# Kernel optimization log

Hardware: AMD Instinct MI355X
Metric: run time of the kernel (lower is better)

Reference implementation:

```python
import jax, jax.numpy as jnp
import numpy as np

E = 16          # expert_num
T = 8192        # token_num
H = 1024        # hidden_size
I = 4096        # intermediate_size
LN_EPS = 1e-12


def setup_inputs() -> dict:
    key = jax.random.key(0)
    ks = jax.random.split(key, 6)
    hidden_states = jax.random.normal(ks[0], (T, H), dtype=jnp.float32)
    perm = jax.random.permutation(ks[1], T).astype(jnp.int32)
    s1 = 1.0 / np.sqrt(H)
    s2 = 1.0 / np.sqrt(I)
    w1 = jax.random.uniform(ks[2], (E, I, H), jnp.float32, -s1, s1)
    b1 = jax.random.uniform(ks[3], (E, I), jnp.float32, -s1, s1)
    w2 = jax.random.uniform(ks[4], (E, H, I), jnp.float32, -s2, s2)
    b2 = jax.random.uniform(ks[5], (E, H), jnp.float32, -s2, s2)
    ln_gamma = jnp.ones((H,), jnp.float32)
    ln_beta = jnp.zeros((H,), jnp.float32)
    return {"hidden_states": hidden_states, "perm": perm, "w1": w1, "b1": b1,
            "w2": w2, "b2": b2, "ln_gamma": ln_gamma, "ln_beta": ln_beta}


def _layer_norm(x, gamma, beta, eps):
    mu = jnp.mean(x, axis=-1, keepdims=True)
    var = jnp.var(x, axis=-1, keepdims=True)
    return (x - mu) * jax.lax.rsqrt(var + eps) * gamma + beta


def reference(hidden_states, perm, w1, b1, w2, b2, ln_gamma, ln_beta):
    # dispatch: gather tokens by random permutation, group per expert
    xp = hidden_states[perm].reshape(E, T // E, H)            # [E, T/E, H]
    # grouped expert FFN (batched GEMM replaces the per-expert Python loop)
    h = jnp.einsum('eth,eih->eti', xp, w1) + b1[:, None, :]   # [E, T/E, I]
    h = jax.nn.gelu(h, approximate=False)
    o = jnp.einsum('eti,ehi->eth', h, w2) + b2[:, None, :]    # [E, T/E, H]
    # scatter-restore via inverse permutation
    restore = jnp.argsort(perm)
    o = o.reshape(T, H)[restore]
    # dropout is identity (p=0, eval); residual + LayerNorm
    return _layer_norm(o + hidden_states, ln_gamma, ln_beta, LN_EPS)
```

## Files before the change

### kernel.cpp

```cpp
#include <hip/hip_runtime.h>
#include <hip/hip_bf16.h>
#include <stdint.h>

#define E_NUM 16
#define T_NUM 8192
#define H_DIM 1024
#define I_DIM 4096
#define MPE   512

typedef __attribute__((ext_vector_type(8))) short short8;
typedef __attribute__((ext_vector_type(4))) float f32x4;
using bf16 = __hip_bfloat16;

typedef const __attribute__((address_space(1))) void GLV;
typedef __attribute__((address_space(3))) void LDSV;

__device__ __forceinline__ uint32_t pack2_bf16(float a, float b) {
  union { float f; uint32_t u; } ua, ub;
  ua.f = a; ub.f = b;
  uint32_t x = ua.u + (0x7FFFu + ((ua.u >> 16) & 1u));
  uint32_t y = ub.u + (0x7FFFu + ((ub.u >> 16) & 1u));
  return (x >> 16) | (y & 0xFFFF0000u);
}

__device__ __forceinline__ short8 cvt8(f32x4 a, f32x4 b) {
  union { short8 s; __hip_bfloat162 h[4]; } r;
  r.h[0] = __float22bfloat162_rn({a[0], a[1]});
  r.h[1] = __float22bfloat162_rn({a[2], a[3]});
  r.h[2] = __float22bfloat162_rn({b[0], b[1]});
  r.h[3] = __float22bfloat162_rn({b[2], b[3]});
  return r.s;
}

__device__ __forceinline__ float fast_gelu(float x) {
  const float p = x * fmaf(x * x, -0.0713548162726f, -1.59576912161f);
  return x * __builtin_amdgcn_rcpf(1.0f + __expf(p));
}

__global__ __launch_bounds__(256)
void gather_cast_kernel(const float* __restrict__ hs, const int* __restrict__ perm,
                        uint32_t* __restrict__ xp) {
  const int r = blockIdx.x;
  const int t = threadIdx.x;
  const int src = perm[r];
  float4 v = ((const float4*)(hs + (size_t)src * H_DIM))[t];
  uint2 o;
  o.x = pack2_bf16(v.x, v.y);
  o.y = pack2_bf16(v.z, v.w);
  ((uint2*)(xp + (size_t)r * (H_DIM / 2)))[t] = o;
}

template<int LOG_NBN, int NWG>
__global__ __launch_bounds__(1024, 2)
void moe_gemm1_kernel(const bf16* __restrict__ A, const float* __restrict__ Bw,
                      const float* __restrict__ bias, bf16* __restrict__ Hout) {
  constexpr int N = I_DIM, K = H_DIM;
  constexpr int NK = K / 32;
  __shared__ bf16  As[2][512 * 32];
  __shared__ float Bs[2][64 * 32];

  constexpr int qx = NWG >> 3;
  const int orig = blockIdx.x;
  const int wg = (orig & 7) * qx + (orig >> 3);
  const int bn = wg & ((1 << LOG_NBN) - 1);
  const int e  = wg >> LOG_NBN;

  const int tid = threadIdx.x;
  const int l = tid & 63;
  const int w = tid >> 6;
  const int wr = w >> 1, wc = w & 1;
  const int fr = l & 15, fq = l >> 4;
  const int rx = fr & 7;

  const bf16*  Ae = A  + (size_t)e * MPE * K;
  const float* Be = Bw + ((size_t)e * N + (size_t)bn * 64) * K;

  const int apq = tid >> 3;
  const int ag  = (tid & 7) ^ (apq & 7);
  const bf16* As0 = Ae + (size_t)(apq       + 256 * (ag >> 2)) * K + (ag & 3) * 8;
  const bf16* As1 = Ae + (size_t)(apq + 128 + 256 * (ag >> 2)) * K + (ag & 3) * 8;

  const int brow = tid >> 3;
  const float* Bsrc = Be + (size_t)(brow & 63) * K + ((tid & 7) ^ (brow & 7)) * 4;

#define STAGE1(buf, kt)                                                            \
  {                                                                                \
    __builtin_amdgcn_global_load_lds((GLV*)(As0 + (kt) * 32),                      \
        (LDSV*)((char*)&As[buf][0] + tid * 16), 16, 0, 0);                         \
    __builtin_amdgcn_global_load_lds((GLV*)(As1 + (kt) * 32),                      \
        (LDSV*)((char*)&As[buf][0] + 16384 + tid * 16), 16, 0, 0);                 \
    if (tid < 512)                                                                 \
      __builtin_amdgcn_global_load_lds((GLV*)(Bsrc + (kt) * 32),                   \
          (LDSV*)((char*)&Bs[buf][0] + tid * 16), 16, 0, 0);                       \
  }

  const int aoff  = ((wr & 3) * 64 + fr) * 128 + ((((wr >> 2) << 2) | fq) ^ rx) * 16;
  const int b0off = (wc * 32 + fr) * 128 + (((fq << 1)) ^ rx) * 16;
  const int b1off = (wc * 32 + fr) * 128 + (((fq << 1) | 1) ^ rx) * 16;

  f32x4 acc[4][2];
#pragma unroll
  for (int m = 0; m < 4; ++m)
#pragma unroll
    for (int n = 0; n < 2; ++n) acc[m][n] = (f32x4){0.f, 0.f, 0.f, 0.f};

  STAGE1(0, 0);
  __syncthreads();

  for (int t = 0; t < NK; ++t) {
    const int cur = t & 1;
    if (t + 1 < NK) STAGE1(cur ^ 1, t + 1);

    short8 a8[4];
#pragma unroll
    for (int m = 0; m < 4; ++m)
      a8[m] = *(const short8*)((const char*)&As[cur][0] + aoff + m * 2048);
    short8 b8[2];
#pragma unroll
    for (int n = 0; n < 2; ++n) {
      const f32x4 x0 = *(const f32x4*)((const char*)&Bs[cur][0] + b0off + n * 2048);
      const f32x4 x1 = *(const f32x4*)((const char*)&Bs[cur][0] + b1off + n * 2048);
      b8[n] = cvt8(x0, x1);
    }
#pragma unroll
    for (int m = 0; m < 4; ++m)
#pragma unroll
      for (int n = 0; n < 2; ++n)
        acc[m][n] = __builtin_amdgcn_mfma_f32_16x16x32_bf16(a8[m], b8[n], acc[m][n], 0, 0, 0);

    __syncthreads();
  }
#undef STAGE1

  float bv[2];
#pragma unroll
  for (int n = 0; n < 2; ++n)
    bv[n] = bias[(size_t)e * N + bn * 64 + wc * 32 + n * 16 + fr];

  bf16* He = Hout + (size_t)e * MPE * N;
#pragma unroll
  for (int m = 0; m < 4; ++m) {
#pragma unroll
    for (int j = 0; j < 4; ++j) {
      const int row = wr * 64 + m * 16 + fq * 4 + j;
#pragma unroll
      for (int n = 0; n < 2; ++n) {
        const int col = bn * 64 + wc * 32 + n * 16 + fr;
        He[(size_t)row * N + col] = __float2bfloat16(fast_gelu(acc[m][n][j] + bv[n]));
      }
    }
  }
}

template<int KSPLIT, int N, int KFULL, int KLEN, int LOG_NBN>
__global__ __launch_bounds__(1024, 4)
void moe_gemm2_kernel(const bf16* __restrict__ A, const float* __restrict__ Bw,
                      float* __restrict__ Pout) {
  constexpr int NK = KLEN / 32;
  __shared__ bf16  As[2][512 * 32];
  __shared__ float Bs[2][128 * 32];

  const int nwg = gridDim.x, qx = nwg >> 3, orig = blockIdx.x;
  const int wg = (orig & 7) * qx + (orig >> 3);
  const int bn   = wg & ((1 << LOG_NBN) - 1);
  const int rest = wg >> LOG_NBN;
  const int ks = (KSPLIT == 2) ? (rest & 1) : 0;
  const int e  = (KSPLIT == 2) ? (rest >> 1) : rest;
  const int K0 = ks * KLEN;

  const int tid = threadIdx.x;
  const int l = tid & 63;
  const int w = tid >> 6;
  const int wr = w >> 1, wc = w & 1;
  const int fr = l & 15, fq = l >> 4;
  const int rx = fr & 7;

  const bf16*  Ae = A  + (size_t)e * MPE * KFULL + K0;
  const float* Be = Bw + ((size_t)e * N + (size_t)bn * 128) * KFULL + K0;

  const int apq = tid >> 3;
  const int ag  = (tid & 7) ^ (apq & 7);
  const bf16* As0 = Ae + (size_t)(apq       + 256 * (ag >> 2)) * KFULL + (ag & 3) * 8;
  const bf16* As1 = Ae + (size_t)(apq + 128 + 256 * (ag >> 2)) * KFULL + (ag & 3) * 8;
  const float* Bsrc = Be + (size_t)(tid >> 3) * KFULL + ((tid & 7) ^ ((tid >> 3) & 7)) * 4;

  const int aso = (((((wr >> 2) << 2)) | fq) ^ rx) * 8;
  const int bp0 = (((fq << 1))     ^ rx) * 4;
  const int bp1 = (((fq << 1) | 1) ^ rx) * 4;

#define STAGE2(buf, kt)                                                             \
  {                                                                                 \
    __builtin_amdgcn_global_load_lds((GLV*)(As0 + (kt) * 32),                       \
                                     (LDSV*)&As[buf][tid * 8], 16, 0, 0);           \
    __builtin_amdgcn_global_load_lds((GLV*)(As1 + (kt) * 32),                       \
                                     (LDSV*)&As[buf][(1024 + tid) * 8], 16, 0, 0);  \
    __builtin_amdgcn_global_load_lds((GLV*)(Bsrc + (kt) * 32),                      \
                                     (LDSV*)&Bs[buf][tid * 4], 16, 0, 0);           \
  }

  f32x4 acc[4][4];
#pragma unroll
  for (int m = 0; m < 4; ++m)
#pragma unroll
    for (int n = 0; n < 4; ++n) acc[m][n] = (f32x4){0.f, 0.f, 0.f, 0.f};

  STAGE2(0, 0);
  __syncthreads();

  for (int t = 0; t < NK; ++t) {
    const int cur = t & 1;
    if (t + 1 < NK) STAGE2(cur ^ 1, t + 1);

    short8 a8[4];
#pragma unroll
    for (int m = 0; m < 4; ++m)
      a8[m] = *(const short8*)&As[cur][((wr & 3) * 64 + m * 16 + fr) * 64 + aso];
#pragma unroll
    for (int n = 0; n < 4; ++n) {
      const int col = wc * 64 + n * 16 + fr;
      const f32x4 x0 = *(const f32x4*)&Bs[cur][col * 32 + bp0];
      const f32x4 x1 = *(const f32x4*)&Bs[cur][col * 32 + bp1];
      const short8 b8 = cvt8(x0, x1);
#pragma unroll
      for (int m = 0; m < 4; ++m)
        acc[m][n] = __builtin_amdgcn_mfma_f32_16x16x32_bf16(a8[m], b8, acc[m][n], 0, 0, 0);
    }
    __syncthreads();
  }
#undef STAGE2

  float* Pd = Pout + (size_t)ks * T_NUM * H_DIM + (size_t)e * MPE * N;
#pragma unroll
  for (int m = 0; m < 4; ++m) {
#pragma unroll
    for (int j = 0; j < 4; ++j) {
      const int row = wr * 64 + m * 16 + fq * 4 + j;
#pragma unroll
      for (int n = 0; n < 4; ++n) {
        const int col = bn * 128 + wc * 64 + n * 16 + fr;
        Pd[(size_t)row * N + col] = acc[m][n][j];
      }
    }
  }
}

__global__ __launch_bounds__(256)
void ln_resid2_kernel(float* __restrict__ out, const float* __restrict__ hs,
                      const float* __restrict__ p0, const float* __restrict__ p1,
                      const float* __restrict__ b2, const float* __restrict__ gamma,
                      const float* __restrict__ beta, const int* __restrict__ perm,
                      const int two) {
  const int r = blockIdx.x;
  const int t = threadIdx.x;
  const int e = r >> 9;
  const int drow = perm[r];
  float4 a = ((const float4*)(p0 + (size_t)r * H_DIM))[t];
  if (two) {
    float4 b = ((const float4*)(p1 + (size_t)r * H_DIM))[t];
    a.x += b.x; a.y += b.y; a.z += b.z; a.w += b.w;
  }
  float4 bb = ((const float4*)(b2 + (size_t)e * H_DIM))[t];
  float4 h  = ((const float4*)(hs + (size_t)drow * H_DIM))[t];
  float v0 = a.x + bb.x + h.x, v1 = a.y + bb.y + h.y;
  float v2 = a.z + bb.z + h.z, v3 = a.w + bb.w + h.w;
  float s  = v0 + v1 + v2 + v3;
  float sq = v0 * v0 + v1 * v1 + v2 * v2 + v3 * v3;
#pragma unroll
  for (int off = 32; off > 0; off >>= 1) {
    s  += __shfl_down(s, off);
    sq += __shfl_down(sq, off);
  }
  __shared__ float ss[4], ssq[4];
  const int wv = t >> 6;
  if ((t & 63) == 0) { ss[wv] = s; ssq[wv] = sq; }
  __syncthreads();
  s  = ss[0] + ss[1] + ss[2] + ss[3];
  sq = ssq[0] + ssq[1] + ssq[2] + ssq[3];
  const float mu  = s * (1.0f / (float)H_DIM);
  const float var = sq * (1.0f / (float)H_DIM) - mu * mu;
  const float rs  = rsqrtf(var + 1e-12f);
  float4 g = ((const float4*)gamma)[t];
  float4 b = ((const float4*)beta)[t];
  float4 rr;
  rr.x = (v0 - mu) * rs * g.x + b.x;
  rr.y = (v1 - mu) * rs * g.y + b.y;
  rr.z = (v2 - mu) * rs * g.z + b.z;
  rr.w = (v3 - mu) * rs * g.w + b.w;
  ((float4*)(out + (size_t)drow * H_DIM))[t] = rr;
}

extern "C" void kernel_launch(void* const* d_in, const int* in_sizes, int n_in,
                              void* d_out, int out_size, void* d_ws, size_t ws_size,
                              hipStream_t stream) {
  const float* hs    = (const float*)d_in[0];
  const int*   perm  = (const int*)d_in[1];
  const float* w1    = (const float*)d_in[2];
  const float* b1    = (const float*)d_in[3];
  const float* w2    = (const float*)d_in[4];
  const float* b2    = (const float*)d_in[5];
  const float* gamma = (const float*)d_in[6];
  const float* beta  = (const float*)d_in[7];
  float* out = (float*)d_out;

  const size_t xp_b   = (size_t)T_NUM * H_DIM * sizeof(bf16);
  const size_t hbuf_b = (size_t)T_NUM * I_DIM * sizeof(bf16);
  const size_t part_b = (size_t)T_NUM * H_DIM * sizeof(float);

  bf16*  xp   = (bf16*)d_ws;
  bf16*  hbuf = (bf16*)((char*)d_ws + xp_b);
  float* pbuf = (float*)((char*)d_ws + xp_b + hbuf_b);

  gather_cast_kernel<<<T_NUM, 256, 0, stream>>>(hs, perm, (uint32_t*)xp);

  moe_gemm1_kernel<6, 1024><<<1024, 1024, 0, stream>>>(xp, w1, b1, hbuf);

  if (ws_size >= xp_b + hbuf_b + 2 * part_b) {
    moe_gemm2_kernel<2, H_DIM, I_DIM, I_DIM / 2, 3>
        <<<256, 1024, 0, stream>>>(hbuf, w2, pbuf);
    ln_resid2_kernel<<<T_NUM, 256, 0, stream>>>(out, hs, pbuf, pbuf + (size_t)T_NUM * H_DIM,
                                                b2, gamma, beta, perm, 1);
  } else {
    moe_gemm2_kernel<1, H_DIM, I_DIM, I_DIM, 3>
        <<<128, 1024, 0, stream>>>(hbuf, w2, pbuf);
    ln_resid2_kernel<<<T_NUM, 256, 0, stream>>>(out, hs, pbuf, nullptr,
                                                b2, gamma, beta, perm, 0);
  }
}
```

Baseline: 344.4 us.

## Retile expert GEMM1 to 256x128 tiles with 512-thread workgroups

The first expert GEMM goes from a 512x64 output tile per 1024-thread workgroup to a 256x128 tile per 512-thread workgroup. The token dimension is now split in two (bm) and each wave accumulates a 4x4 grid of MFMA tiles instead of 4x2. Each workgroup streams less of the activation matrix, fp32 weights are reused across fewer rows, and each B fragment converted from fp32 to bf16 feeds more MFMAs. In exchange, accumulator register pressure roughly doubles per thread, and the A operand is re-read by two workgroups per expert.

```diff
diff --git a/kernel.cpp b/kernel.cpp
--- a/kernel.cpp
+++ b/kernel.cpp
@@ -51,58 +51,59 @@
 }
 
 template<int LOG_NBN, int NWG>
-__global__ __launch_bounds__(1024, 2)
-void moe_gemm1_kernel(const bf16* __restrict__ A, const float* __restrict__ Bw,
-                      const float* __restrict__ bias, bf16* __restrict__ Hout) {
+__global__ __launch_bounds__(512, 2)
+void moe_g1_kernel(const bf16* __restrict__ A, const float* __restrict__ Bw,
+                   const float* __restrict__ bias, bf16* __restrict__ Hout) {
   constexpr int N = I_DIM, K = H_DIM;
   constexpr int NK = K / 32;
-  __shared__ bf16  As[2][512 * 32];
-  __shared__ float Bs[2][64 * 32];
+  __shared__ bf16  As[2][128 * 64];
+  __shared__ float Bs[2][128 * 32];
 
   constexpr int qx = NWG >> 3;
   const int orig = blockIdx.x;
   const int wg = (orig & 7) * qx + (orig >> 3);
-  const int bn = wg & ((1 << LOG_NBN) - 1);
-  const int e  = wg >> LOG_NBN;
+  const int bm = wg & 1;
+  const int bn = (wg >> 1) & ((1 << LOG_NBN) - 1);
+  const int e  = wg >> (1 + LOG_NBN);
 
   const int tid = threadIdx.x;
   const int l = tid & 63;
-  const int w = tid >> 6;
-  const int wr = w >> 1, wc = w & 1;
+  const int wv = tid >> 6;
+  const int wr = wv >> 1, wc = wv & 1;
   const int fr = l & 15, fq = l >> 4;
   const int rx = fr & 7;
 
-  const bf16*  Ae = A  + (size_t)e * MPE * K;
-  const float* Be = Bw + ((size_t)e * N + (size_t)bn * 64) * K;
-
-  const int apq = tid >> 3;
-  const int ag  = (tid & 7) ^ (apq & 7);
-  const bf16* As0 = Ae + (size_t)(apq       + 256 * (ag >> 2)) * K + (ag & 3) * 8;
-  const bf16* As1 = Ae + (size_t)(apq + 128 + 256 * (ag >> 2)) * K + (ag & 3) * 8;
-
-  const int brow = tid >> 3;
-  const float* Bsrc = Be + (size_t)(brow & 63) * K + ((tid & 7) ^ (brow & 7)) * 4;
+  const bf16*  Ae = A  + ((size_t)e * MPE + (size_t)bm * 256) * K;
+  const float* Be = Bw + ((size_t)e * N + (size_t)bn * 128) * K;
+
+  const int p0 = tid >> 3;
+  const int ga = (tid & 7) ^ (p0 & 7);
+  const bf16* As0 = Ae + (size_t)(p0      + 128 * (ga >> 2)) * K + (ga & 3) * 8;
+  const bf16* As1 = Ae + (size_t)(p0 + 64 + 128 * (ga >> 2)) * K + (ga & 3) * 8;
+  const float* Bs0 = Be + (size_t)p0 * K + ga * 4;
+  const float* Bs1 = Be + (size_t)(p0 + 64) * K + ga * 4;
 
 #define STAGE1(buf, kt)                                                            \
   {                                                                                \
     __builtin_amdgcn_global_load_lds((GLV*)(As0 + (kt) * 32),                      \
         (LDSV*)((char*)&As[buf][0] + tid * 16), 16, 0, 0);                         \
     __builtin_amdgcn_global_load_lds((GLV*)(As1 + (kt) * 32),                      \
-        (LDSV*)((char*)&As[buf][0] + 16384 + tid * 16), 16, 0, 0);                 \
-    if (tid < 512)                                                                 \
-      __builtin_amdgcn_global_load_lds((GLV*)(Bsrc + (kt) * 32),                   \
-          (LDSV*)((char*)&Bs[buf][0] + tid * 16), 16, 0, 0);                       \
-  }
-
-  const int aoff  = ((wr & 3) * 64 + fr) * 128 + ((((wr >> 2) << 2) | fq) ^ rx) * 16;
-  const int b0off = (wc * 32 + fr) * 128 + (((fq << 1)) ^ rx) * 16;
-  const int b1off = (wc * 32 + fr) * 128 + (((fq << 1) | 1) ^ rx) * 16;
-
-  f32x4 acc[4][2];
+        (LDSV*)((char*)&As[buf][0] + 8192 + tid * 16), 16, 0, 0);                  \
+    __builtin_amdgcn_global_load_lds((GLV*)(Bs0 + (kt) * 32),                      \
+        (LDSV*)((char*)&Bs[buf][0] + tid * 16), 16, 0, 0);                         \
+    __builtin_amdgcn_global_load_lds((GLV*)(Bs1 + (kt) * 32),                      \
+        (LDSV*)((char*)&Bs[buf][0] + 8192 + tid * 16), 16, 0, 0);                  \
+  }
+
+  const int aoff  = ((wr & 1) * 64 + fr) * 128 + ((((wr >> 1) << 2) | fq) ^ rx) * 16;
+  const int b0off = (wc * 64 + fr) * 128 + (((fq << 1)) ^ rx) * 16;
+  const int b1off = (wc * 64 + fr) * 128 + (((fq << 1) | 1) ^ rx) * 16;
+
+  f32x4 acc[4][4];
 #pragma unroll
   for (int m = 0; m < 4; ++m)
 #pragma unroll
-    for (int n = 0; n < 2; ++n) acc[m][n] = (f32x4){0.f, 0.f, 0.f, 0.f};
+    for (int n = 0; n < 4; ++n) acc[m][n] = (f32x4){0.f, 0.f, 0.f, 0.f};
 
   STAGE1(0, 0);
   __syncthreads();
@@ -115,9 +116,9 @@
 #pragma unroll
     for (int m = 0; m < 4; ++m)
       a8[m] = *(const short8*)((const char*)&As[cur][0] + aoff + m * 2048);
-    short8 b8[2];
-#pragma unroll
-    for (int n = 0; n < 2; ++n) {
+    short8 b8[4];
+#pragma unroll
+    for (int n = 0; n < 4; ++n) {
       const f32x4 x0 = *(const f32x4*)((const char*)&Bs[cur][0] + b0off + n * 2048);
       const f32x4 x1 = *(const f32x4*)((const char*)&Bs[cur][0] + b1off + n * 2048);
       b8[n] = cvt8(x0, x1);
@@ -125,27 +126,27 @@
 #pragma unroll
     for (int m = 0; m < 4; ++m)
 #pragma unroll
-      for (int n = 0; n < 2; ++n)
+      for (int n = 0; n < 4; ++n)
         acc[m][n] = __builtin_amdgcn_mfma_f32_16x16x32_bf16(a8[m], b8[n], acc[m][n], 0, 0, 0);
 
     __syncthreads();
   }
 #undef STAGE1
 
-  float bv[2];
-#pragma unroll
-  for (int n = 0; n < 2; ++n)
-    bv[n] = bias[(size_t)e * N + bn * 64 + wc * 32 + n * 16 + fr];
+  float bv[4];
+#pragma unroll
+  for (int n = 0; n < 4; ++n)
+    bv[n] = bias[(size_t)e * N + bn * 128 + wc * 64 + n * 16 + fr];
 
   bf16* He = Hout + (size_t)e * MPE * N;
 #pragma unroll
   for (int m = 0; m < 4; ++m) {
 #pragma unroll
     for (int j = 0; j < 4; ++j) {
-      const int row = wr * 64 + m * 16 + fq * 4 + j;
-#pragma unroll
-      for (int n = 0; n < 2; ++n) {
-        const int col = bn * 64 + wc * 32 + n * 16 + fr;
+      const int row = bm * 256 + wr * 64 + m * 16 + fq * 4 + j;
+#pragma unroll
+      for (int n = 0; n < 4; ++n) {
+        const int col = bn * 128 + wc * 64 + n * 16 + fr;
         He[(size_t)row * N + col] = __float2bfloat16(fast_gelu(acc[m][n][j] + bv[n]));
       }
     }
@@ -154,8 +155,8 @@
 
 template<int KSPLIT, int N, int KFULL, int KLEN, int LOG_NBN>
 __global__ __launch_bounds__(1024, 4)
-void moe_gemm2_kernel(const bf16* __restrict__ A, const float* __restrict__ Bw,
-                      float* __restrict__ Pout) {
+void moe_g2_kernel(const bf16* __restrict__ A, const float* __restrict__ Bw,
+                   float* __restrict__ Pout) {
   constexpr int NK = KLEN / 32;
   __shared__ bf16  As[2][512 * 32];
   __shared__ float Bs[2][128 * 32];
@@ -312,15 +313,15 @@
 
   gather_cast_kernel<<<T_NUM, 256, 0, stream>>>(hs, perm, (uint32_t*)xp);
 
-  moe_gemm1_kernel<6, 1024><<<1024, 1024, 0, stream>>>(xp, w1, b1, hbuf);
+  moe_g1_kernel<5, 1024><<<1024, 512, 0, stream>>>(xp, w1, b1, hbuf);
 
   if (ws_size >= xp_b + hbuf_b + 2 * part_b) {
-    moe_gemm2_kernel<2, H_DIM, I_DIM, I_DIM / 2, 3>
+    moe_g2_kernel<2, H_DIM, I_DIM, I_DIM / 2, 3>
         <<<256, 1024, 0, stream>>>(hbuf, w2, pbuf);
     ln_resid2_kernel<<<T_NUM, 256, 0, stream>>>(out, hs, pbuf, pbuf + (size_t)T_NUM * H_DIM,
                                                 b2, gamma, beta, perm, 1);
   } else {
-    moe_gemm2_kernel<1, H_DIM, I_DIM, I_DIM, 3>
+    moe_g2_kernel<1, H_DIM, I_DIM, I_DIM, 3>
         <<<128, 1024, 0, stream>>>(hbuf, w2, pbuf);
     ln_resid2_kernel<<<T_NUM, 256, 0, stream>>>(out, hs, pbuf, nullptr,
                                                 b2, gamma, beta, perm, 0);
```

Result: faster. 331.8 us (-3.7%).
